# Kernel optimization log

Hardware: AMD Instinct MI355X
Metric: run time of the kernel (lower is better)

The kernel has to match this reference:

```python
import jax, jax.numpy as jnp
import numpy as np

B, MAXT, MAXU, A = 16, 200, 101, 512
BLANK = 0


def setup_inputs() -> dict:
    key = jax.random.key(0)
    k1, k2, k3, k4 = jax.random.split(key, 4)
    logits = jax.random.normal(k1, (B, MAXT, MAXU, A), dtype=jnp.float32)
    log_probs = jax.nn.log_softmax(logits, axis=-1)  # transducer expects log-softmaxed acts
    labels = jax.random.randint(k2, (B, MAXU - 1), 1, A, dtype=jnp.int32)  # non-blank targets
    T = jax.random.randint(k3, (B,), MAXT // 2, MAXT + 1, dtype=jnp.int32)  # frames per utt
    U = jax.random.randint(k4, (B,), (MAXU - 1) // 2, MAXU, dtype=jnp.int32)  # labels per utt, <= MAXU-1
    return {"log_probs": log_probs, "labels": labels, "T": T, "U": U}


def _alpha_lattice(blk, emit):
    """RNN-T forward variables.
    blk, emit: [B, T, U] log-probs of blank / correct label at each lattice cell.
    Recurrence: alpha[t,u] = logaddexp(alpha[t-1,u]+blk[t-1,u], alpha[t,u-1]+emit[t,u-1]).
    Within a time step the u-recursion is solved in closed form with a
    log-cumsum-exp (associative_scan of logaddexp), so the only sequential
    loop is the scan over t.
    """
    Bb, Tm, Um = blk.shape

    def prefix_emit(emit_t):  # c[u] = sum_{k<u} emit_t[k]
        return jnp.concatenate(
            [jnp.zeros((Bb, 1), emit_t.dtype), jnp.cumsum(emit_t[:, :-1], axis=1)], axis=1)

    alpha0 = prefix_emit(emit[:, 0])  # alpha[0,u] = sum of first u emits, alpha[0,0]=0

    def step(alpha_prev, inputs):
        blk_tm1, emit_t = inputs            # [B, U] each
        a = alpha_prev + blk_tm1            # no-emit entry point per u
        c = prefix_emit(emit_t)
        # alpha[t,u] = c[u] + LSE_{u'<=u}(a[u'] - c[u'])
        alpha_t = c + jax.lax.associative_scan(jnp.logaddexp, a - c, axis=1)
        return alpha_t, alpha_t

    xs = (jnp.moveaxis(blk[:, :-1], 1, 0), jnp.moveaxis(emit[:, 1:], 1, 0))
    _, rest = jax.lax.scan(step, alpha0, xs)          # [T-1, B, U]
    alpha = jnp.concatenate([alpha0[None], rest], axis=0)  # [T, B, U]
    return jnp.moveaxis(alpha, 0, 1)                  # [B, T, U]


def reference(log_probs, labels, T, U):
    Bb, Tm, Um, _ = log_probs.shape
    blk = log_probs[..., BLANK]                       # [B, T, U]
    lab = jnp.concatenate([labels, jnp.zeros((Bb, 1), labels.dtype)], axis=1)  # pad to [B, U]
    idx = jnp.broadcast_to(lab[:, None, :, None], (Bb, Tm, Um, 1))
    emit = jnp.take_along_axis(log_probs, idx, axis=3)[..., 0]  # log P(label_u | t, u)
    alpha = _alpha_lattice(blk, emit)
    bidx = jnp.arange(Bb)
    # log_p = alpha[T-1, U] + blank emission at terminal cell (== beta[0,0])
    log_p = alpha[bidx, T - 1, U] + blk[bidx, T - 1, U]
    return jnp.mean(-log_p)  # reduction='mean'; -(lpa+lpb)/2 == -log_p exactly
```

## Files before the change

### kernel.cpp

```cpp
#include <hip/hip_runtime.h>
#include <math.h>


#define BATCH 16
#define TMAX  200
#define UMAX  101
#define VOC   512
#define NDIAG (TMAX + UMAX - 1)
#define PITCH 128
#define DEPTH 8
#define NEGINF (-INFINITY)

__device__ __forceinline__ float lse2(float a, float b) {
    float m = fmaxf(a, b);
    float r = m + __logf(__expf(a - m) + __expf(b - m));
    return (m == NEGINF) ? NEGINF : r;
}

__global__ __launch_bounds__(PITCH) void gather_kernel(
    const float* __restrict__ lp, const int* __restrict__ labels,
    float* __restrict__ Dblk, float* __restrict__ Demit)
{
    const int d = blockIdx.x;
    const int b = blockIdx.y;
    const int u = threadIdx.x;
    const size_t row = ((size_t)b * NDIAG + d) * PITCH + u;

    const int tt = d - u - 1;
    float vb = NEGINF;
    if (u < UMAX && tt >= 0 && tt < TMAX)
        vb = lp[(((size_t)b * TMAX + tt) * UMAX + u) * VOC];

    const int te = d - u;
    float ve = NEGINF;
    if (u >= 1 && u < UMAX && te >= 0 && te < TMAX) {
        const int lab = labels[b * (UMAX - 1) + (u - 1)];
        ve = lp[(((size_t)b * TMAX + te) * UMAX + (u - 1)) * VOC + lab];
    }
    Dblk[row]  = vb;
    Demit[row] = ve;
}

__global__ __launch_bounds__(64) void sweep_kernel(
    const float* __restrict__ Dblk, const float* __restrict__ Demit,
    const float* __restrict__ lp,
    const int* __restrict__ Tarr, const int* __restrict__ Uarr,
    float* __restrict__ out)
{
    const int b    = blockIdx.x;
    const int lane = threadIdx.x;
    const int Tb   = Tarr[b];
    const int Ub   = Uarr[b];
    const int dmax = Tb - 1 + Ub;

    const float2* rb = (const float2*)(Dblk  + (size_t)b * NDIAG * PITCH);
    const float2* re = (const float2*)(Demit + (size_t)b * NDIAG * PITCH);

    float A0 = (lane == 0) ? 0.0f : NEGINF;
    float A1 = NEGINF;

    float2 qb[DEPTH], qe[DEPTH];
#pragma unroll
    for (int j = 0; j < DEPTH; ++j) {
        int d = min(1 + j, dmax);
        qb[j] = rb[d * 64 + lane];
        qe[j] = re[d * 64 + lane];
    }

    for (int dbase = 1; dbase <= dmax; dbase += DEPTH) {
        float2 cb[DEPTH], ce[DEPTH];
#pragma unroll
        for (int j = 0; j < DEPTH; ++j) { cb[j] = qb[j]; ce[j] = qe[j]; }
#pragma unroll
        for (int j = 0; j < DEPTH; ++j) {
            int dn = min(dbase + DEPTH + j, dmax);
            qb[j] = rb[dn * 64 + lane];
            qe[j] = re[dn * 64 + lane];
        }
#pragma unroll
        for (int j = 0; j < DEPTH; ++j) {
            if (dbase + j > dmax) break;
            float Aup = __shfl_up(A1, 1);
            float n0 = lse2(A0 + cb[j].x, Aup + ce[j].x);
            float n1 = lse2(A1 + cb[j].y, A0  + ce[j].y);
            A0 = n0; A1 = n1;
        }
    }

    if (lane == (Ub >> 1)) {
        float Af   = (Ub & 1) ? A1 : A0;
        float blkf = lp[(((size_t)b * TMAX + (Tb - 1)) * UMAX + Ub) * VOC];
        atomicAdd(out, -(Af + blkf) * (1.0f / BATCH));
    }
}

extern "C" void kernel_launch(void* const* d_in, const int* in_sizes, int n_in,
                              void* d_out, int out_size, void* d_ws, size_t ws_size,
                              hipStream_t stream) {
    const float* lp     = (const float*)d_in[0];
    const int*   labels = (const int*)d_in[1];
    const int*   Tarr   = (const int*)d_in[2];
    const int*   Uarr   = (const int*)d_in[3];
    float* out = (float*)d_out;

    float* Dblk  = (float*)d_ws;
    float* Demit = Dblk + (size_t)BATCH * NDIAG * PITCH;

    hipMemsetAsync(out, 0, sizeof(float), stream);

    dim3 g1(NDIAG, BATCH);
    gather_kernel<<<g1, PITCH, 0, stream>>>(lp, labels, Dblk, Demit);
    sweep_kernel<<<BATCH, 64, 0, stream>>>(Dblk, Demit, lp, Tarr, Uarr, out);
}
```

Baseline: 755.5 us.

## Interleave blank/emit diagonals into float4 slots and double-buffer sweep prefetch

```diff
diff --git a/kernel.cpp b/kernel.cpp
--- a/kernel.cpp
+++ b/kernel.cpp
@@ -7,9 +7,10 @@
 #define UMAX  101
 #define VOC   512
 #define NDIAG (TMAX + UMAX - 1)
-#define PITCH 128
 #define DEPTH 8
 #define NEGINF (-INFINITY)
+
+#define SLOTS 64
 
 __device__ __forceinline__ float lse2(float a, float b) {
     float m = fmaxf(a, b);
@@ -17,33 +18,38 @@
     return (m == NEGINF) ? NEGINF : r;
 }
 
-__global__ __launch_bounds__(PITCH) void gather_kernel(
+__global__ __launch_bounds__(256) void init_kernel(float4* __restrict__ F) {
+    const size_t i = (size_t)blockIdx.x * 256 + threadIdx.x;
+    F[i] = make_float4(NEGINF, NEGINF, NEGINF, NEGINF);
+}
+
+__global__ __launch_bounds__(128) void gather_kernel(
     const float* __restrict__ lp, const int* __restrict__ labels,
-    float* __restrict__ Dblk, float* __restrict__ Demit)
+    float* __restrict__ F)
 {
-    const int d = blockIdx.x;
+    const int t = blockIdx.x;
     const int b = blockIdx.y;
     const int u = threadIdx.x;
-    const size_t row = ((size_t)b * NDIAG + d) * PITCH + u;
+    if (u >= UMAX) return;
 
-    const int tt = d - u - 1;
-    float vb = NEGINF;
-    if (u < UMAX && tt >= 0 && tt < TMAX)
-        vb = lp[(((size_t)b * TMAX + tt) * UMAX + u) * VOC];
+    const size_t rowbase = (((size_t)b * TMAX + t) * UMAX + u) * VOC;
+    const int d = t + u + 1;
+    float* Fb = F + (size_t)b * NDIAG * (SLOTS * 4);
 
-    const int te = d - u;
-    float ve = NEGINF;
-    if (u >= 1 && u < UMAX && te >= 0 && te < TMAX) {
-        const int lab = labels[b * (UMAX - 1) + (u - 1)];
-        ve = lp[(((size_t)b * TMAX + te) * UMAX + (u - 1)) * VOC + lab];
+    if (d < NDIAG) {
+        const float vb = lp[rowbase];
+        Fb[(size_t)d * (SLOTS * 4) + (u >> 1) * 4 + (u & 1)] = vb;
     }
-    Dblk[row]  = vb;
-    Demit[row] = ve;
+    if (u < UMAX - 1) {
+        const int lab = labels[b * (UMAX - 1) + u];
+        const float ve = lp[rowbase + lab];
+        const int uc = u + 1;
+        Fb[(size_t)d * (SLOTS * 4) + (uc >> 1) * 4 + 2 + (uc & 1)] = ve;
+    }
 }
 
 __global__ __launch_bounds__(64) void sweep_kernel(
-    const float* __restrict__ Dblk, const float* __restrict__ Demit,
-    const float* __restrict__ lp,
+    const float4* __restrict__ F, const float* __restrict__ lp,
     const int* __restrict__ Tarr, const int* __restrict__ Uarr,
     float* __restrict__ out)
 {
@@ -53,38 +59,45 @@
     const int Ub   = Uarr[b];
     const int dmax = Tb - 1 + Ub;
 
-    const float2* rb = (const float2*)(Dblk  + (size_t)b * NDIAG * PITCH);
-    const float2* re = (const float2*)(Demit + (size_t)b * NDIAG * PITCH);
+    const float4* rf = F + (size_t)b * NDIAG * SLOTS + lane;
 
     float A0 = (lane == 0) ? 0.0f : NEGINF;
     float A1 = NEGINF;
 
-    float2 qb[DEPTH], qe[DEPTH];
+    float4 qa[DEPTH], qb[DEPTH];
 #pragma unroll
-    for (int j = 0; j < DEPTH; ++j) {
-        int d = min(1 + j, dmax);
-        qb[j] = rb[d * 64 + lane];
-        qe[j] = re[d * 64 + lane];
-    }
+    for (int j = 0; j < DEPTH; ++j)
+        qa[j] = rf[(size_t)min(1 + j, dmax) * SLOTS];
+#pragma unroll
+    for (int j = 0; j < DEPTH; ++j)
+        qb[j] = rf[(size_t)min(1 + DEPTH + j, dmax) * SLOTS];
 
-    for (int dbase = 1; dbase <= dmax; dbase += DEPTH) {
-        float2 cb[DEPTH], ce[DEPTH];
-#pragma unroll
-        for (int j = 0; j < DEPTH; ++j) { cb[j] = qb[j]; ce[j] = qe[j]; }
-#pragma unroll
-        for (int j = 0; j < DEPTH; ++j) {
-            int dn = min(dbase + DEPTH + j, dmax);
-            qb[j] = rb[dn * 64 + lane];
-            qe[j] = re[dn * 64 + lane];
-        }
+    for (int dbase = 1; dbase <= dmax; dbase += 2 * DEPTH) {
 #pragma unroll
         for (int j = 0; j < DEPTH; ++j) {
             if (dbase + j > dmax) break;
+            const float4 q = qa[j];
             float Aup = __shfl_up(A1, 1);
-            float n0 = lse2(A0 + cb[j].x, Aup + ce[j].x);
-            float n1 = lse2(A1 + cb[j].y, A0  + ce[j].y);
+            float n0 = lse2(A0 + q.x, Aup + q.y * 0.0f + Aup * 0.0f + q.z + Aup);
+            n0 = lse2(A0 + q.x, Aup + q.z);
+            float n1 = lse2(A1 + q.y, A0 + q.w);
             A0 = n0; A1 = n1;
         }
+#pragma unroll
+        for (int j = 0; j < DEPTH; ++j)
+            qa[j] = rf[(size_t)min(dbase + 2 * DEPTH + j, dmax) * SLOTS];
+#pragma unroll
+        for (int j = 0; j < DEPTH; ++j) {
+            if (dbase + DEPTH + j > dmax) break;
+            const float4 q = qb[j];
+            float Aup = __shfl_up(A1, 1);
+            float n0 = lse2(A0 + q.x, Aup + q.z);
+            float n1 = lse2(A1 + q.y, A0 + q.w);
+            A0 = n0; A1 = n1;
+        }
+#pragma unroll
+        for (int j = 0; j < DEPTH; ++j)
+            qb[j] = rf[(size_t)min(dbase + 3 * DEPTH + j, dmax) * SLOTS];
     }
 
     if (lane == (Ub >> 1)) {
@@ -103,12 +116,15 @@
     const int*   Uarr   = (const int*)d_in[3];
     float* out = (float*)d_out;
 
-    float* Dblk  = (float*)d_ws;
-    float* Demit = Dblk + (size_t)BATCH * NDIAG * PITCH;
+    float4* F = (float4*)d_ws;
 
     hipMemsetAsync(out, 0, sizeof(float), stream);
 
-    dim3 g1(NDIAG, BATCH);
-    gather_kernel<<<g1, PITCH, 0, stream>>>(lp, labels, Dblk, Demit);
-    sweep_kernel<<<BATCH, 64, 0, stream>>>(Dblk, Demit, lp, Tarr, Uarr, out);
+    const int n_f4 = BATCH * NDIAG * SLOTS;
+    init_kernel<<<n_f4 / 256, 256, 0, stream>>>(F);
+
+    dim3 g1(TMAX, BATCH);
+    gather_kernel<<<g1, 128, 0, stream>>>(lp, labels, (float*)F);
+
+    sweep_kernel<<<BATCH, 64, 0, stream>>>(F, lp, Tarr, Uarr, out);
 }
```

After: 763.4 us. Within noise of the previous version (+1.0%).
